# Kernel tuning notes

Hardware: AMD Instinct MI355X
Metric: run time of the kernel (lower is better)

## Reference

```python
import jax, jax.numpy as jnp
import numpy as np
import math

B, NRES, RPR = 1, 384, 3
L = NRES * RPR          # 1152 rigids
CS, CZ = 256, 128
CH, H, PQ, PV = 16, 8, 8, 12


def _ln(x, scale, bias):
    mu = jnp.mean(x, axis=-1, keepdims=True)
    var = jnp.var(x, axis=-1, keepdims=True)
    return (x - mu) * jax.lax.rsqrt(var + 1e-5) * scale + bias


def _quat_to_rot(q):
    q = q / jnp.linalg.norm(q, axis=-1, keepdims=True)
    w, x, y, z = q[..., 0], q[..., 1], q[..., 2], q[..., 3]
    r = jnp.stack([
        1 - 2 * (y * y + z * z), 2 * (x * y - w * z), 2 * (x * z + w * y),
        2 * (x * y + w * z), 1 - 2 * (x * x + z * z), 2 * (y * z - w * x),
        2 * (x * z - w * y), 2 * (y * z + w * x), 1 - 2 * (x * x + y * y),
    ], axis=-1)
    return r.reshape(q.shape[:-1] + (3, 3))


def setup_inputs() -> dict:
    key = jax.random.key(0)
    ks = jax.random.split(key, 20)
    s = jax.random.normal(ks[0], (B, L, CS), jnp.float32)
    z = jax.random.normal(ks[1], (B, NRES, NRES, CZ), jnp.float32)
    rot = _quat_to_rot(jax.random.normal(ks[2], (B, L, 4), jnp.float32))
    trans = 10.0 * jax.random.normal(ks[3], (B, L, 3), jnp.float32)
    mask = jnp.ones((B, L), jnp.float32)
    rigid_to_res_idx = jnp.broadcast_to(jnp.arange(L, dtype=jnp.int32) // RPR, (B, L))
    w = lambda k, sh: 0.02 * jax.random.normal(k, sh, jnp.float32)
    return {
        "s": s, "z": z, "rot": rot, "trans": trans, "mask": mask,
        "ln_s_scale": jnp.ones((CS,), jnp.float32), "ln_s_bias": jnp.zeros((CS,), jnp.float32),
        "ln_z_scale": jnp.ones((CZ,), jnp.float32), "ln_z_bias": jnp.zeros((CZ,), jnp.float32),
        "w_q": w(ks[4], (CS, H * CH)), "w_k": w(ks[5], (CS, H * CH)), "w_v": w(ks[6], (CS, H * CH)),
        "w_qp": w(ks[7], (CS, H * PQ * 3)), "w_kp": w(ks[8], (CS, H * PQ * 3)), "w_vp": w(ks[9], (CS, H * PV * 3)),
        "w_b": w(ks[10], (CZ, H)),
        "head_weights": jnp.full((H,), 0.5413, jnp.float32),  # softplus^-1(1)
        "w_out": w(ks[11], (H * (CH + CZ + PV * 4), CS)),
        "b_out": jnp.zeros((CS,), jnp.float32),
        "rigid_to_res_idx": rigid_to_res_idx,
    }


def reference(s, z, rot, trans, mask, ln_s_scale, ln_s_bias, ln_z_scale, ln_z_bias,
              w_q, w_k, w_v, w_qp, w_kp, w_vp, w_b, head_weights, w_out, b_out,
              rigid_to_res_idx):
    b_, l_ = s.shape[0], s.shape[1]
    idx = rigid_to_res_idx[0]                       # [L] rigid -> residue, shared over batch
    s_ln = _ln(s, ln_s_scale, ln_s_bias)            # [B,L,CS]
    z_ln = _ln(z, ln_z_scale, ln_z_bias)            # [B,N,N,CZ]

    q = (s_ln @ w_q).reshape(b_, l_, H, CH)
    k = (s_ln @ w_k).reshape(b_, l_, H, CH)
    v = (s_ln @ w_v).reshape(b_, l_, H, CH)

    # local points, then rigid-transform to global frame: x_g = R x + t
    q_p = (s_ln @ w_qp).reshape(b_, l_, H, PQ, 3)
    k_p = (s_ln @ w_kp).reshape(b_, l_, H, PQ, 3)
    v_p = (s_ln @ w_vp).reshape(b_, l_, H, PV, 3)
    t5 = trans[:, :, None, None, :]
    q_g = jnp.einsum("blij,blhpj->blhpi", rot, q_p) + t5
    k_g = jnp.einsum("blij,blhpj->blhpi", rot, k_p) + t5
    v_g = jnp.einsum("blij,blhpj->blhpi", rot, v_p) + t5

    # scalar qk term
    a = jnp.einsum("blhc,bjhc->bhlj", q, k) * math.sqrt(1.0 / (3 * CH))
    # pair bias, broadcast residue-pair -> rigid-pair
    b_res = z_ln @ w_b                                # [B,N,N,H]
    b_full = b_res[:, idx][:, :, idx]                 # [B,L,L,H]
    a = a + math.sqrt(1.0 / 3) * jnp.transpose(b_full, (0, 3, 1, 2))
    # point-distance term: ||q-k||^2 = |q|^2 + |k|^2 - 2 q.k (summed over P,3)
    hw = jax.nn.softplus(head_weights) * math.sqrt(1.0 / (3 * (PQ * 9.0 / 2)))
    qq = jnp.sum(q_g * q_g, axis=(-1, -2)).transpose(0, 2, 1)   # [B,H,L]
    kk = jnp.sum(k_g * k_g, axis=(-1, -2)).transpose(0, 2, 1)
    qk = jnp.einsum("blhpc,bjhpc->bhlj", q_g, k_g)
    d2 = qq[:, :, :, None] + kk[:, :, None, :] - 2.0 * qk
    a = a - 0.5 * d2 * hw[None, :, None, None]
    a = a + (mask[:, None, None, :] - 1.0) * 1e9
    attn = jax.nn.softmax(a, axis=-1)                 # [B,H,L,L]

    o = jnp.einsum("bhlj,bjhc->blhc", attn, v)        # [B,L,H,CH]
    o_pt_g = jnp.einsum("bhlj,bjhpc->blhpc", attn, v_g)
    # back to local frame of query rigid: R^T (x - t)
    o_pt = jnp.einsum("blji,blhpj->blhpi", rot, o_pt_g - t5)
    o_pt_norm = jnp.sqrt(jnp.sum(o_pt * o_pt, axis=-1) + 1e-8)  # [B,L,H,PV]
    # pair output: sum attention over rigids belonging to each key residue
    attn_res = attn.reshape(b_, H, l_, NRES, RPR).sum(-1)       # [B,H,L,N]
    z_l = z_ln[:, idx]                                           # [B,L,N,CZ]
    o_pair = jnp.einsum("bhln,blnc->blhc", attn_res, z_l)        # [B,L,H,CZ]

    cat = jnp.concatenate(
        [o, o_pt.reshape(b_, l_, H, PV * 3), o_pt_norm, o_pair], axis=-1
    ).reshape(b_, l_, H * (CH + PV * 4 + CZ))
    return cat @ w_out + b_out                        # [B,L,CS]
```

## Files before the change

### kernel.cpp

```cpp
#include <hip/hip_runtime.h>
#include <hip/hip_bf16.h>

#define L 1152
#define NRES 384
#define CS 256
#define CZ 128
#define H 8
#define CH 16
#define PQ 8
#define PV 12
#define PSTR 1088

#define OFF_SLN  0L
#define OFF_PROJ 294912L
#define OFF_WPK  1548288L
#define OFF_QCAT 1826816L
#define OFF_KCAT 2232320L
#define OFF_VCAT 2637824L
#define OFF_BRES 3227648L
#define OFF_MURS 4407296L
#define OFF_ATTN 4702208L
#define OFF_CAT  15319040L
#define OFF_PAV  18286592L
#define OFF_POP  21825536L
#define OFF_ARES 26544128L
#define OFF_PCAT 30083072L

__global__ __launch_bounds__(256) void k_pre(
    const float* wq, const float* wk, const float* wv,
    const float* wqp, const float* wkp, const float* wvp, float* wpack,
    const float* s, const float* lnss, const float* lnsb, float* sln,
    const float* z, const float* lnzs, const float* lnzb,
    const float* wb, float* murs, float* bres_t){
  int bx = blockIdx.x, t = threadIdx.x;
  if(bx < 256){
    int k = bx;
    for(int c=t; c<PSTR; c+=256){
      float v;
      if(c<128)        v = wq [(long)k*128 + c];
      else if(c<256)   v = wk [(long)k*128 + c-128];
      else if(c<384)   v = wv [(long)k*128 + c-256];
      else if(c<576)   v = wqp[(long)k*192 + c-384];
      else if(c<768)   v = wkp[(long)k*192 + c-576];
      else if(c<1056)  v = wvp[(long)k*288 + c-768];
      else             v = 0.f;
      wpack[(long)k*PSTR + c] = v;
    }
    return;
  }
  if(bx < 256 + L){
    int l = bx - 256;
    __shared__ float red[CS];
    float x = s[(long)l*CS + t];
    red[t] = x; __syncthreads();
    for(int st=128; st>0; st>>=1){ if(t<st) red[t]+=red[t+st]; __syncthreads(); }
    float mu = red[0] * (1.f/CS); __syncthreads();
    float d = x - mu;
    red[t] = d*d; __syncthreads();
    for(int st=128; st>0; st>>=1){ if(t<st) red[t]+=red[t+st]; __syncthreads(); }
    float var = red[0]*(1.f/CS);
    sln[(long)l*CS + t] = d*rsqrtf(var + 1e-5f)*lnss[t] + lnsb[t];
    return;
  }
  {
    long rp0 = (long)(bx - 256 - L)*32;
    int r = t>>3, part = t&7;
    long rp = rp0 + r;
    __shared__ __align__(16) float swb[8*132];
    __shared__ float SB[8][2];
    const float4* z4 = (const float4*)z;
    float4 x0 = z4[rp*32 + part*4 + 0];
    float4 x1 = z4[rp*32 + part*4 + 1];
    float4 x2 = z4[rp*32 + part*4 + 2];
    float4 x3 = z4[rp*32 + part*4 + 3];
    #pragma unroll
    for(int k2=0;k2<4;k2++){
      int e = t + k2*256; int h = e>>7, c = e&127;
      swb[h*132 + c] = lnzs[c]*wb[(long)c*8 + h];
    }
    __syncthreads();
    if(t < 64){
      int h = t>>3, seg = t&7;
      float S=0, Bv=0;
      #pragma unroll
      for(int i=0;i<16;i++){
        int c = seg*16+i;
        S  += swb[h*132+c];
        Bv += lnzb[c]*wb[(long)c*8 + h];
      }
      #pragma unroll
      for(int off=1;off<8;off<<=1){ S += __shfl_xor(S,off,64); Bv += __shfl_xor(Bv,off,64); }
      if(seg==0){ SB[h][0]=S; SB[h][1]=Bv; }
    }
    float s1 = x0.x+x0.y+x0.z+x0.w + x1.x+x1.y+x1.z+x1.w
             + x2.x+x2.y+x2.z+x2.w + x3.x+x3.y+x3.z+x3.w;
    float s2 = x0.x*x0.x+x0.y*x0.y+x0.z*x0.z+x0.w*x0.w
             + x1.x*x1.x+x1.y*x1.y+x1.z*x1.z+x1.w*x1.w
             + x2.x*x2.x+x2.y*x2.y+x2.z*x2.z+x2.w*x2.w
             + x3.x*x3.x+x3.y*x3.y+x3.z*x3.z+x3.w*x3.w;
    #pragma unroll
    for(int off=1;off<8;off<<=1){ s1 += __shfl_xor(s1,off,64); s2 += __shfl_xor(s2,off,64); }
    float mu = s1*(1.f/CZ);
    float var = s2*(1.f/CZ) - mu*mu;
    float rstd = rsqrtf(var + 1e-5f);
    if(part==0){ murs[rp*2]=mu; murs[rp*2+1]=rstd; }
    float acc[8];
    const float4* swb4 = (const float4*)swb;
    #pragma unroll
    for(int h=0;h<8;h++){
      float4 wa = swb4[h*33 + part*4 + 0];
      float4 wbv= swb4[h*33 + part*4 + 1];
      float4 wc = swb4[h*33 + part*4 + 2];
      float4 wd = swb4[h*33 + part*4 + 3];
      acc[h] = x0.x*wa.x + x0.y*wa.y + x0.z*wa.z + x0.w*wa.w
             + x1.x*wbv.x+ x1.y*wbv.y+ x1.z*wbv.z+ x1.w*wbv.w
             + x2.x*wc.x + x2.y*wc.y + x2.z*wc.z + x2.w*wc.w
             + x3.x*wd.x + x3.y*wd.y + x3.z*wd.z + x3.w*wd.w;
    }
    #pragma unroll
    for(int off=1;off<8;off<<=1){
      #pragma unroll
      for(int h=0;h<8;h++) acc[h] += __shfl_xor(acc[h],off,64);
    }
    __syncthreads();
    if(part==0){
      #pragma unroll
      for(int h=0;h<8;h++)
        bres_t[(long)h*147456 + rp] = rstd*(acc[h] - mu*SB[h][0]) + SB[h][1];
    }
  }
}

__global__ __launch_bounds__(256) void k_proj(const float* sln, const float* wpack, float* proj){
  int l0 = blockIdx.x*64, c0 = blockIdx.y*64, t = threadIdx.x;
  __shared__ float a_s[32][68];
  __shared__ __align__(16) float w_s[32][68];
  int tr = t>>4, tc = t&15;
  float4 acc[4] = {{0,0,0,0},{0,0,0,0},{0,0,0,0},{0,0,0,0}};
  for(int kc=0; kc<8; kc++){
    int k0 = kc*32;
    {
      int row = t>>2, kk0 = (t&3)*8;
      const float4* src = (const float4*)(sln + (long)(l0+row)*256 + k0 + kk0);
      float4 v0 = src[0], v1 = src[1];
      a_s[kk0+0][row]=v0.x; a_s[kk0+1][row]=v0.y; a_s[kk0+2][row]=v0.z; a_s[kk0+3][row]=v0.w;
      a_s[kk0+4][row]=v1.x; a_s[kk0+5][row]=v1.y; a_s[kk0+6][row]=v1.z; a_s[kk0+7][row]=v1.w;
    }
    #pragma unroll
    for(int kk2=0; kk2<2; kk2++){
      int kk = (t>>4) + 16*kk2;
      *(float4*)&w_s[kk][(t&15)*4] = *(const float4*)(wpack + (long)(k0+kk)*PSTR + c0 + (t&15)*4);
    }
    __syncthreads();
    #pragma unroll 8
    for(int kk=0; kk<32; kk++){
      float4 a4 = *(const float4*)&a_s[kk][tr*4];
      float4 b4 = *(const float4*)&w_s[kk][tc*4];
      acc[0].x+=a4.x*b4.x; acc[0].y+=a4.x*b4.y; acc[0].z+=a4.x*b4.z; acc[0].w+=a4.x*b4.w;
      acc[1].x+=a4.y*b4.x; acc[1].y+=a4.y*b4.y; acc[1].z+=a4.y*b4.z; acc[1].w+=a4.y*b4.w;
      acc[2].x+=a4.z*b4.x; acc[2].y+=a4.z*b4.y; acc[2].z+=a4.z*b4.z; acc[2].w+=a4.z*b4.w;
      acc[3].x+=a4.w*b4.x; acc[3].y+=a4.w*b4.y; acc[3].z+=a4.w*b4.z; acc[3].w+=a4.w*b4.w;
    }
    __syncthreads();
  }
  #pragma unroll
  for(int r=0;r<4;r++)
    *(float4*)(proj + (long)(l0 + tr*4 + r)*PSTR + c0 + tc*4) = acc[r];
}

__global__ __launch_bounds__(256) void k_rigid(const float* proj, const float* rot, const float* trans,
                        const float* mask, const float* hws,
                        float* qcat, float* kcat, float* vcat){
  int l = blockIdx.x, t = threadIdx.x;
  __shared__ float R[9], T[3], hwS[8], qgs[192], kgs[192];
  if(t<9) R[t]=rot[(long)l*9+t];
  if(t<3) T[t]=trans[(long)l*3+t];
  if(t>=16 && t<24) hwS[t-16] = log1pf(expf(hws[t-16]))*0.09622504486493764f;
  __syncthreads();
  const float* pr = proj + (long)l*PSTR;
  if(t<128){
    int h=t>>4, c=t&15;
    long base = ((long)h*L + l)*44;
    qcat[base + c] = 0.14433756729740643f * pr[t];
    kcat[base + c] = pr[128+t];
    vcat[((long)h*L + l)*64 + c] = pr[256+t];
  }
  if(t < 192){
    int h=t/24, m=t%24, p=m/3, i=m%3;
    float qa = R[i*3+0]*pr[384+h*24+p*3+0] + R[i*3+1]*pr[384+h*24+p*3+1]
             + R[i*3+2]*pr[384+h*24+p*3+2] + T[i];
    float ka = R[i*3+0]*pr[576+h*24+p*3+0] + R[i*3+1]*pr[576+h*24+p*3+1]
             + R[i*3+2]*pr[576+h*24+p*3+2] + T[i];
    qgs[t]=qa; kgs[t]=ka;
    long base = ((long)h*L + l)*44 + 16 + m;
    qcat[base] = hwS[h]*qa;
    kcat[base] = ka;
  }
  for(int it=t; it<288; it+=256){
    int h=it/36, m=it%36, p=m/3, i=m%3;
    float a = R[i*3+0]*pr[768+h*36+p*3+0] + R[i*3+1]*pr[768+h*36+p*3+1]
            + R[i*3+2]*pr[768+h*36+p*3+2] + T[i];
    vcat[((long)h*L + l)*64 + 16 + m] = a;
  }
  if(t < 96){
    int h=t/12, d=t%12;
    vcat[((long)h*L + l)*64 + 52 + d] = 0.f;
  }
  __syncthreads();
  if(t < 8){
    float qq=0, kk=0;
    #pragma unroll
    for(int m=0;m<24;m++){ qq += qgs[t*24+m]*qgs[t*24+m]; kk += kgs[t*24+m]*kgs[t*24+m]; }
    long base = ((long)t*L + l)*44;
    qcat[base + 40] = -0.5f*hwS[t]*qq;
    kcat[base + 40] = -0.5f*hwS[t]*kk + (mask[l]-1.f)*1e9f;
  }
}

__global__ __launch_bounds__(256) void k_scores(const float* qcat, const float* kcat,
                         const float* bres_t, const int* ridx, float* attn){
  int l0 = blockIdx.x*32, j0 = blockIdx.y*64, h = blockIdx.z;
  int t = threadIdx.x;
  __shared__ __align__(16) float q_s[32*44];
  __shared__ __align__(16) float k_s[64*44];
  __shared__ int rj_s[64];
  {
    const float* srcq = qcat + ((long)h*L + l0)*44;
    for(int i=t; i<32*44; i+=256) q_s[i]=srcq[i];
    const float* srck = kcat + ((long)h*L + j0)*44;
    for(int i=t; i<64*44; i+=256) k_s[i]=srck[i];
    if(t<64) rj_s[t]=ridx[j0+t];
  }
  __syncthreads();
  int a = t>>5;
  int b = t&31;
  float acc[4][2] = {{0,0},{0,0},{0,0},{0,0}};
  const float4* q4 = (const float4*)q_s;
  const float4* k4 = (const float4*)k_s;
  #pragma unroll
  for(int i=0;i<10;i++){
    float4 kA = k4[(long)b*11 + i];
    float4 kB = k4[(long)(b+32)*11 + i];
    #pragma unroll
    for(int r=0;r<4;r++){
      float4 qv = q4[(long)(a+8*r)*11 + i];
      acc[r][0] += qv.x*kA.x + qv.y*kA.y + qv.z*kA.z + qv.w*kA.w;
      acc[r][1] += qv.x*kB.x + qv.y*kB.y + qv.z*kB.z + qv.w*kB.w;
    }
  }
  float colc0 = k_s[b*44+40], colc1 = k_s[(b+32)*44+40];
  int rj0 = rj_s[b], rj1 = rj_s[b+32];
  const float* bbh = bres_t + (long)h*147456;
  #pragma unroll
  for(int r=0;r<4;r++){
    int row = a+8*r;
    float rowc = q_s[row*44+40];
    int rl = ridx[l0+row];
    const float* bb = bbh + (long)rl*NRES;
    float s0 = acc[r][0] + rowc + colc0 + 0.5773502691896258f*bb[rj0];
    float s1 = acc[r][1] + rowc + colc1 + 0.5773502691896258f*bb[rj1];
    float* arow = attn + ((long)h*L + l0+row)*L + j0;
    arow[b]    = s0;
    arow[b+32] = s1;
  }
}

__global__ __launch_bounds__(256) void k_rowstat(float* attn, float* ares){
  long row = (long)blockIdx.x*4 + (threadIdx.x>>6);
  int lane = threadIdx.x & 63;
  int w = threadIdx.x >> 6;
  __shared__ float es[4][1152];
  float* p = attn + row*L;
  float v[18];
  float m=-1e30f;
  #pragma unroll
  for(int i=0;i<18;i++){ v[i]=p[lane + i*64]; m=fmaxf(m,v[i]); }
  #pragma unroll
  for(int off=1;off<64;off<<=1) m=fmaxf(m,__shfl_xor(m,off,64));
  float s=0;
  #pragma unroll
  for(int i=0;i<18;i++){ v[i]=__expf(v[i]-m); s+=v[i]; }
  #pragma unroll
  for(int off=1;off<64;off<<=1) s+=__shfl_xor(s,off,64);
  float inv = 1.f/s;
  #pragma unroll
  for(int i=0;i<18;i++){
    float pv = v[i]*inv;
    p[lane + i*64] = pv;
    es[w][lane + i*64] = pv;
  }
  __syncthreads();
  #pragma unroll
  for(int q=0;q<6;q++){
    int n = lane + q*64;
    ares[row*NRES + n] = es[w][3*n] + es[w][3*n+1] + es[w][3*n+2];
  }
}

__global__ __launch_bounds__(256) void k_av(const float* attn, const float* vcat, float* pav){
  int lb = blockIdx.x, h = blockIdx.y, sp = blockIdx.z, t = threadIdx.x;
  int l0 = lb*64;
  __shared__ __align__(16) float a_s[64][68];
  __shared__ __align__(16) float v_s[64][68];
  int lgrp = t>>4, dgrp = t&15;
  float4 acc[4] = {{0,0,0,0},{0,0,0,0},{0,0,0,0},{0,0,0,0}};
  const float* abase = attn + ((long)h*L + l0)*L;
  int al = t>>2, jj0s = (t&3)*16;
  for(int jc=sp*3; jc<sp*3+3; jc++){
    int j0 = jc*64;
    {
      const float4* src = (const float4*)(abase + (long)al*L + j0 + jj0s);
      float4 p0 = src[0], p1 = src[1], p2 = src[2], p3 = src[3];
      a_s[jj0s+ 0][al]=p0.x; a_s[jj0s+ 1][al]=p0.y; a_s[jj0s+ 2][al]=p0.z; a_s[jj0s+ 3][al]=p0.w;
      a_s[jj0s+ 4][al]=p1.x; a_s[jj0s+ 5][al]=p1.y; a_s[jj0s+ 6][al]=p1.z; a_s[jj0s+ 7][al]=p1.w;
      a_s[jj0s+ 8][al]=p2.x; a_s[jj0s+ 9][al]=p2.y; a_s[jj0s+10][al]=p2.z; a_s[jj0s+11][al]=p2.w;
      a_s[jj0s+12][al]=p3.x; a_s[jj0s+13][al]=p3.y; a_s[jj0s+14][al]=p3.z; a_s[jj0s+15][al]=p3.w;
    }
    {
      int jj = t>>2, seg = t&3;
      const float4* src = (const float4*)(vcat + ((long)h*L + j0 + jj)*64 + seg*16);
      float4 q0=src[0], q1=src[1], q2=src[2], q3=src[3];
      float4* dst = (float4*)&v_s[jj][seg*16];
      dst[0]=q0; dst[1]=q1; dst[2]=q2; dst[3]=q3;
    }
    __syncthreads();
    #pragma unroll 8
    for(int jj=0; jj<64; jj++){
      float4 av = *(const float4*)&a_s[jj][lgrp*4];
      float4 vv = *(const float4*)&v_s[jj][dgrp*4];
      acc[0].x+=av.x*vv.x; acc[0].y+=av.x*vv.y; acc[0].z+=av.x*vv.z; acc[0].w+=av.x*vv.w;
      acc[1].x+=av.y*vv.x; acc[1].y+=av.y*vv.y; acc[1].z+=av.y*vv.z; acc[1].w+=av.y*vv.w;
      acc[2].x+=av.z*vv.x; acc[2].y+=av.z*vv.y; acc[2].z+=av.z*vv.z; acc[2].w+=av.z*vv.w;
      acc[3].x+=av.w*vv.x; acc[3].y+=av.w*vv.y; acc[3].z+=av.w*vv.z; acc[3].w+=av.w*vv.w;
    }
    __syncthreads();
  }
  #pragma unroll
  for(int r=0;r<4;r++)
    *(float4*)(pav + (((long)sp*H + h)*L + l0 + lgrp*4 + r)*64 + dgrp*4) = acc[r];
}

#define OPAIR_STEP(Z0,Z1,Z2,Z3,NB) { \
    float4 a0 = *(const float4*)&ar[0][th][NB]; \
    float4 a1 = *(const float4*)&ar[1][th][NB]; \
    float4 a2 = *(const float4*)&ar[2][th][NB]; \
    acc[0][0] += a0.x*Z0.x + a0.y*Z1.x + a0.z*Z2.x + a0.w*Z3.x; \
    acc[0][1] += a0.x*Z0.y + a0.y*Z1.y + a0.z*Z2.y + a0.w*Z3.y; \
    acc[0][2] += a0.x*Z0.z + a0.y*Z1.z + a0.z*Z2.z + a0.w*Z3.z; \
    acc[0][3] += a0.x*Z0.w + a0.y*Z1.w + a0.z*Z2.w + a0.w*Z3.w; \
    acc[1][0] += a1.x*Z0.x + a1.y*Z1.x + a1.z*Z2.x + a1.w*Z3.x; \
    acc[1][1] += a1.x*Z0.y + a1.y*Z1.y + a1.z*Z2.y + a1.w*Z3.y; \
    acc[1][2] += a1.x*Z0.z + a1.y*Z1.z + a1.z*Z2.z + a1.w*Z3.z; \
    acc[1][3] += a1.x*Z0.w + a1.y*Z1.w + a1.z*Z2.w + a1.w*Z3.w; \
    acc[2][0] += a2.x*Z0.x + a2.y*Z1.x + a2.z*Z2.x + a2.w*Z3.x; \
    acc[2][1] += a2.x*Z0.y + a2.y*Z1.y + a2.z*Z2.y + a2.w*Z3.y; \
    acc[2][2] += a2.x*Z0.z + a2.y*Z1.z + a2.z*Z2.z + a2.w*Z3.z; \
    acc[2][3] += a2.x*Z0.w + a2.y*Z1.w + a2.z*Z2.w + a2.w*Z3.w; }

__global__ __launch_bounds__(256) void k_opair(const float* ares, const float* z, const float* murs,
                        const float* sc, const int* ridx, float* po){
  int r=blockIdx.x, sp=blockIdx.y, t=threadIdx.x;
  __shared__ __align__(16) float ar[3][H][96];
  __shared__ __align__(16) float mrs[96*2];
  __shared__ float S1s[24];
  int rl = ridx[r*3];
  int n0 = sp*96;
  int tc = t&31, th = t>>5;
  const float* zbase = z + ((long)(rl*NRES + n0))*CZ + tc*4;
  float4 zc0 = *(const float4*)(zbase + 0L*CZ);
  float4 zc1 = *(const float4*)(zbase + 1L*CZ);
  float4 zc2 = *(const float4*)(zbase + 2L*CZ);
  float4 zc3 = *(const float4*)(zbase + 3L*CZ);
  for(int i=t;i<192;i+=256) mrs[i]=murs[((long)rl*NRES + n0)*2 + i];
  __syncthreads();
  for(int it=t; it<3*H*96; it+=256){
    int lo = it/(H*96);
    int rem = it - lo*(H*96);
    int h = rem/96, n = rem - h*96;
    ar[lo][h][n] = ares[((long)h*L + r*3+lo)*NRES + n0 + n] * mrs[n*2+1];
  }
  __syncthreads();
  if(t<192){
    int row=t>>3, seg=t&7;
    const float* arr = ((const float*)ar) + row*96 + seg*12;
    const float* mur = mrs + seg*24;
    float s1=0;
    #pragma unroll
    for(int q2=0;q2<12;q2++) s1 += arr[q2]*mur[q2*2];
    s1 += __shfl_xor(s1,1,64); s1 += __shfl_xor(s1,2,64); s1 += __shfl_xor(s1,4,64);
    if(seg==0) S1s[row]=s1;
  }
  __syncthreads();
  float acc[3][4]={};
  for(int nb=0; nb<88; nb+=8){
    float4 zn0 = *(const float4*)(zbase + (long)(nb+4)*CZ);
    float4 zn1 = *(const float4*)(zbase + (long)(nb+5)*CZ);
    float4 zn2 = *(const float4*)(zbase + (long)(nb+6)*CZ);
    float4 zn3 = *(const float4*)(zbase + (long)(nb+7)*CZ);
    OPAIR_STEP(zc0,zc1,zc2,zc3, nb);
    zc0 = *(const float4*)(zbase + (long)(nb+ 8)*CZ);
    zc1 = *(const float4*)(zbase + (long)(nb+ 9)*CZ);
    zc2 = *(const float4*)(zbase + (long)(nb+10)*CZ);
    zc3 = *(const float4*)(zbase + (long)(nb+11)*CZ);
    OPAIR_STEP(zn0,zn1,zn2,zn3, nb+4);
  }
  {
    float4 zn0 = *(const float4*)(zbase + 92L*CZ);
    float4 zn1 = *(const float4*)(zbase + 93L*CZ);
    float4 zn2 = *(const float4*)(zbase + 94L*CZ);
    float4 zn3 = *(const float4*)(zbase + 95L*CZ);
    OPAIR_STEP(zc0,zc1,zc2,zc3, 88);
    OPAIR_STEP(zn0,zn1,zn2,zn3, 92);
  }
  float4 sc4 = *(const float4*)(sc + tc*4);
  #pragma unroll
  for(int lo=0;lo<3;lo++){
    float s1v = S1s[lo*8+th];
    float4 o = { sc4.x*(acc[lo][0]-s1v), sc4.y*(acc[lo][1]-s1v),
                 sc4.z*(acc[lo][2]-s1v), sc4.w*(acc[lo][3]-s1v) };
    *(float4*)(po + ((long)sp*L + (long)(r*3+lo))*1024 + th*128 + tc*4) = o;
  }
}

__global__ __launch_bounds__(256) void k_post(const float* pav, const float* rot, const float* trans,
                        const float* po, const float* bi, float* cat){
  int bx = blockIdx.x, t = threadIdx.x;
  if(bx < 288){
    int lb = bx % 36, h = bx / 36;
    int l0 = lb*32;
    __shared__ __align__(16) float fin_s[32][64];
    #pragma unroll
    for(int k=0;k<2;k++){
      int fi = t + k*256;
      int l = fi>>4, c4 = fi&15;
      long base = (((long)h)*L + l0 + l)*64 + c4*4;
      float4 r = {0,0,0,0};
      #pragma unroll
      for(int p=0;p<6;p++){
        float4 a = *(const float4*)(pav + (long)p*589824 + base);
        r.x+=a.x; r.y+=a.y; r.z+=a.z; r.w+=a.w;
      }
      *(float4*)&fin_s[l][c4*4] = r;
    }
    __syncthreads();
    for(int it=t; it<32*16; it+=256){
      int l=it>>4, c=it&15;
      cat[(long)(l0+l)*1536 + h*192 + c] = fin_s[l][c];
    }
    for(int it=t; it<32*12; it+=256){
      int l=it/12, p=it%12;
      long gl = l0+l;
      float og0 = fin_s[l][16+p*3+0]-trans[gl*3+0];
      float og1 = fin_s[l][16+p*3+1]-trans[gl*3+1];
      float og2 = fin_s[l][16+p*3+2]-trans[gl*3+2];
      float* crow = cat + gl*1536 + h*192;
      float nrm=0;
      #pragma unroll
      for(int i=0;i<3;i++){
        float v = rot[gl*9+0+i]*og0 + rot[gl*9+3+i]*og1 + rot[gl*9+6+i]*og2;
        crow[16+p*3+i]=v; nrm+=v*v;
      }
      crow[52+p]=sqrtf(nrm+1e-8f);
    }
    return;
  }
  {
    int i = (bx-288)*256 + t;
    const float4* p = (const float4*)po;
    float4 a = p[i], b = p[i + 294912], c = p[i + 589824], d = p[i + 884736];
    int l = i>>8, rem = i&255;
    int h = rem>>5, c4 = rem&31;
    float4 bv = ((const float4*)bi)[c4];
    float4 r = {a.x+b.x+c.x+d.x+bv.x, a.y+b.y+c.y+d.y+bv.y,
                a.z+b.z+c.z+d.z+bv.z, a.w+b.w+c.w+d.w+bv.w};
    ((float4*)cat)[(long)l*384 + h*48 + 16 + c4] = r;
  }
}

__global__ __launch_bounds__(256) void k_final(const float* cat, const float* wout, float* pcat){
  int l0 = blockIdx.x*64, c0 = blockIdx.y*64, kp = blockIdx.z, t = threadIdx.x;
  __shared__ __align__(16) float a_s[64][68];
  __shared__ __align__(16) float w_s[64][68];
  int lgrp = t>>4, cgrp = t&15;
  float4 acc[4] = {{0,0,0,0},{0,0,0,0},{0,0,0,0},{0,0,0,0}};
  int al = t>>2, ks0 = (t&3)*16;
  for(int kc=0; kc<3; kc++){
    int k0 = kp*192 + kc*64;
    {
      const float4* src = (const float4*)(cat + (long)(l0+al)*1536 + k0 + ks0);
      float4 p0 = src[0], p1 = src[1], p2 = src[2], p3 = src[3];
      a_s[ks0+ 0][al]=p0.x; a_s[ks0+ 1][al]=p0.y; a_s[ks0+ 2][al]=p0.z; a_s[ks0+ 3][al]=p0.w;
      a_s[ks0+ 4][al]=p1.x; a_s[ks0+ 5][al]=p1.y; a_s[ks0+ 6][al]=p1.z; a_s[ks0+ 7][al]=p1.w;
      a_s[ks0+ 8][al]=p2.x; a_s[ks0+ 9][al]=p2.y; a_s[ks0+10][al]=p2.z; a_s[ks0+11][al]=p2.w;
      a_s[ks0+12][al]=p3.x; a_s[ks0+13][al]=p3.y; a_s[ks0+14][al]=p3.z; a_s[ks0+15][al]=p3.w;
    }
    {
      int kk = t>>2, seg = t&3;
      const float4* src = (const float4*)(wout + (long)(k0+kk)*256 + c0 + seg*16);
      float4 q0=src[0], q1=src[1], q2=src[2], q3=src[3];
      float4* dst = (float4*)&w_s[kk][seg*16];
      dst[0]=q0; dst[1]=q1; dst[2]=q2; dst[3]=q3;
    }
    __syncthreads();
    #pragma unroll 8
    for(int kk=0; kk<64; kk++){
      float4 av = *(const float4*)&a_s[kk][lgrp*4];
      float4 wv = *(const float4*)&w_s[kk][cgrp*4];
      acc[0].x+=av.x*wv.x; acc[0].y+=av.x*wv.y; acc[0].z+=av.x*wv.z; acc[0].w+=av.x*wv.w;
      acc[1].x+=av.y*wv.x; acc[1].y+=av.y*wv.y; acc[1].z+=av.y*wv.z; acc[1].w+=av.y*wv.w;
      acc[2].x+=av.z*wv.x; acc[2].y+=av.z*wv.y; acc[2].z+=av.z*wv.z; acc[2].w+=av.z*wv.w;
      acc[3].x+=av.w*wv.x; acc[3].y+=av.w*wv.y; acc[3].z+=av.w*wv.z; acc[3].w+=av.w*wv.w;
    }
    __syncthreads();
  }
  #pragma unroll
  for(int r=0;r<4;r++)
    *(float4*)(pcat + ((long)kp*L + l0 + lgrp*4 + r)*256 + c0 + cgrp*4) = acc[r];
}

__global__ __launch_bounds__(256) void k_redout(const float* pcat, const float* bout, float* out){
  int i = blockIdx.x*256 + threadIdx.x;
  const float4* p = (const float4*)pcat;
  float4 bv = ((const float4*)bout)[i&63];
  float4 r = bv;
  #pragma unroll
  for(int p8=0;p8<8;p8++){
    float4 a = p[i + (long)p8*73728];
    r.x+=a.x; r.y+=a.y; r.z+=a.z; r.w+=a.w;
  }
  ((float4*)out)[i] = r;
}

extern "C" void kernel_launch(void* const* d_in, const int* in_sizes, int n_in,
                              void* d_out, int out_size, void* d_ws, size_t ws_size,
                              hipStream_t stream) {
  const float* s      = (const float*)d_in[0];
  const float* z      = (const float*)d_in[1];
  const float* rot    = (const float*)d_in[2];
  const float* trans  = (const float*)d_in[3];
  const float* mask   = (const float*)d_in[4];
  const float* lnss   = (const float*)d_in[5];
  const float* lnsb   = (const float*)d_in[6];
  const float* lnzs   = (const float*)d_in[7];
  const float* lnzb   = (const float*)d_in[8];
  const float* wq     = (const float*)d_in[9];
  const float* wk     = (const float*)d_in[10];
  const float* wv     = (const float*)d_in[11];
  const float* wqp    = (const float*)d_in[12];
  const float* wkp    = (const float*)d_in[13];
  const float* wvp    = (const float*)d_in[14];
  const float* wb     = (const float*)d_in[15];
  const float* hws    = (const float*)d_in[16];
  const float* wout   = (const float*)d_in[17];
  const float* bout   = (const float*)d_in[18];
  const int*  ridx    = (const int*)d_in[19];

  float* ws  = (float*)d_ws;
  float* out = (float*)d_out;

  float* sln  = ws + OFF_SLN;
  float* proj = ws + OFF_PROJ;
  float* wpk  = ws + OFF_WPK;
  float* qcat = ws + OFF_QCAT;
  float* kcat = ws + OFF_KCAT;
  float* vcat = ws + OFF_VCAT;
  float* bres = ws + OFF_BRES;
  float* murs = ws + OFF_MURS;
  float* attn = ws + OFF_ATTN;
  float* cat  = ws + OFF_CAT;
  float* pcat = ws + OFF_PCAT;
  float* pav  = ws + OFF_PAV;
  float* po   = ws + OFF_POP;
  float* ares = ws + OFF_ARES;

  k_pre<<<dim3(256 + L + NRES*NRES/32), dim3(256), 0, stream>>>(
      wq, wk, wv, wqp, wkp, wvp, wpk,
      s, lnss, lnsb, sln,
      z, lnzs, lnzb, wb, murs, bres);
  k_proj<<<dim3(18,17), dim3(256), 0, stream>>>(sln, wpk, proj);
  k_rigid<<<dim3(L), dim3(256), 0, stream>>>(proj, rot, trans, mask, hws, qcat, kcat, vcat);
  k_scores<<<dim3(L/32, L/64, H), dim3(256), 0, stream>>>(qcat, kcat, bres, ridx, attn);
  k_rowstat<<<dim3(H*L/4), dim3(256), 0, stream>>>(attn, ares);
  k_av<<<dim3(L/64, H, 6), dim3(256), 0, stream>>>(attn, vcat, pav);
  k_opair<<<dim3(NRES, 4), dim3(256), 0, stream>>>(ares, z, murs, lnzs, ridx, po);
  k_post<<<dim3(288 + 1152), dim3(256), 0, stream>>>(pav, rot, trans, po, lnzb, cat);
  k_final<<<dim3(L/64, 4, 8), dim3(256), 0, stream>>>(cat, wout, pcat);
  k_redout<<<dim3(288), dim3(256), 0, stream>>>(pcat, bout, out);
}
```

Before: 309.1 us.

## Transpose q/k layout and use 4x4 register-tiled score kernel with staged pair bias

Stores the concatenated q and k features channel-major so the score kernel can load transposed tiles and compute a 4x4 outer-product micro-tile per thread over a 32x128 block, writing float4 rows. The pair bias block for the covered residues is staged in shared memory, and the residue index is computed as j/3 instead of read from the index array. This cuts shared-memory traffic per FMA and scattered global bias gathers, but it hardcodes three rigids per residue and makes the rigid kernel's stores strided.

```diff
diff --git a/kernel.cpp b/kernel.cpp
--- a/kernel.cpp
+++ b/kernel.cpp
@@ -180,9 +180,8 @@
   const float* pr = proj + (long)l*PSTR;
   if(t<128){
     int h=t>>4, c=t&15;
-    long base = ((long)h*L + l)*44;
-    qcat[base + c] = 0.14433756729740643f * pr[t];
-    kcat[base + c] = pr[128+t];
+    qcat[((long)h*44 + c)*L + l] = 0.14433756729740643f * pr[t];
+    kcat[((long)h*44 + c)*L + l] = pr[128+t];
     vcat[((long)h*L + l)*64 + c] = pr[256+t];
   }
   if(t < 192){
@@ -192,9 +191,8 @@
     float ka = R[i*3+0]*pr[576+h*24+p*3+0] + R[i*3+1]*pr[576+h*24+p*3+1]
              + R[i*3+2]*pr[576+h*24+p*3+2] + T[i];
     qgs[t]=qa; kgs[t]=ka;
-    long base = ((long)h*L + l)*44 + 16 + m;
-    qcat[base] = hwS[h]*qa;
-    kcat[base] = ka;
+    qcat[((long)h*44 + 16 + m)*L + l] = hwS[h]*qa;
+    kcat[((long)h*44 + 16 + m)*L + l] = ka;
   }
   for(int it=t; it<288; it+=256){
     int h=it/36, m=it%36, p=m/3, i=m%3;
@@ -211,57 +209,66 @@
     float qq=0, kk=0;
     #pragma unroll
     for(int m=0;m<24;m++){ qq += qgs[t*24+m]*qgs[t*24+m]; kk += kgs[t*24+m]*kgs[t*24+m]; }
-    long base = ((long)t*L + l)*44;
-    qcat[base + 40] = -0.5f*hwS[t]*qq;
-    kcat[base + 40] = -0.5f*hwS[t]*kk + (mask[l]-1.f)*1e9f;
+    qcat[((long)t*44 + 40)*L + l] = -0.5f*hwS[t]*qq;
+    kcat[((long)t*44 + 40)*L + l] = -0.5f*hwS[t]*kk + (mask[l]-1.f)*1e9f;
   }
 }
 
 __global__ __launch_bounds__(256) void k_scores(const float* qcat, const float* kcat,
-                         const float* bres_t, const int* ridx, float* attn){
-  int l0 = blockIdx.x*32, j0 = blockIdx.y*64, h = blockIdx.z;
+                         const float* bres_t, float* attn){
+  int l0 = blockIdx.x*32, j0 = blockIdx.y*128, h = blockIdx.z;
   int t = threadIdx.x;
-  __shared__ __align__(16) float q_s[32*44];
-  __shared__ __align__(16) float k_s[64*44];
-  __shared__ int rj_s[64];
+  __shared__ __align__(16) float q_t[44*36];
+  __shared__ __align__(16) float k_t[44*132];
+  __shared__ float bp[12*44];
+  int rl0 = l0/3, rj0 = j0/3;
   {
-    const float* srcq = qcat + ((long)h*L + l0)*44;
-    for(int i=t; i<32*44; i+=256) q_s[i]=srcq[i];
-    const float* srck = kcat + ((long)h*L + j0)*44;
-    for(int i=t; i<64*44; i+=256) k_s[i]=srck[i];
-    if(t<64) rj_s[t]=ridx[j0+t];
-  }
-  __syncthreads();
-  int a = t>>5;
-  int b = t&31;
-  float acc[4][2] = {{0,0},{0,0},{0,0},{0,0}};
-  const float4* q4 = (const float4*)q_s;
-  const float4* k4 = (const float4*)k_s;
-  #pragma unroll
-  for(int i=0;i<10;i++){
-    float4 kA = k4[(long)b*11 + i];
-    float4 kB = k4[(long)(b+32)*11 + i];
-    #pragma unroll
-    for(int r=0;r<4;r++){
-      float4 qv = q4[(long)(a+8*r)*11 + i];
-      acc[r][0] += qv.x*kA.x + qv.y*kA.y + qv.z*kA.z + qv.w*kA.w;
-      acc[r][1] += qv.x*kB.x + qv.y*kB.y + qv.z*kB.z + qv.w*kB.w;
-    }
-  }
-  float colc0 = k_s[b*44+40], colc1 = k_s[(b+32)*44+40];
-  int rj0 = rj_s[b], rj1 = rj_s[b+32];
-  const float* bbh = bres_t + (long)h*147456;
+    const float* srcq = qcat + (long)h*44*L + l0;
+    for(int i=t; i<44*32; i+=256){
+      int c = i>>5, ll = i&31;
+      q_t[c*36 + ll] = srcq[(long)c*L + ll];
+    }
+    const float* srck = kcat + (long)h*44*L + j0;
+    for(int i=t; i<44*128; i+=256){
+      int c = i>>7, jj = i&127;
+      k_t[c*132 + jj] = srck[(long)c*L + jj];
+    }
+    const float* bb = bres_t + (long)h*147456;
+    for(int i=t; i<12*44; i+=256){
+      int r = i/44, c = i-r*44;
+      int rr = rl0+r, cc = rj0+c;
+      bp[i] = (rr<NRES && cc<NRES) ? bb[(long)rr*NRES + cc] : 0.f;
+    }
+  }
+  __syncthreads();
+  int lg = t>>5, jg = t&31;
+  float acc[4][4] = {};
+  #pragma unroll 4
+  for(int c=0;c<40;c++){
+    float4 qv = *(const float4*)&q_t[c*36 + lg*4];
+    float4 kv = *(const float4*)&k_t[c*132 + jg*4];
+    acc[0][0]+=qv.x*kv.x; acc[0][1]+=qv.x*kv.y; acc[0][2]+=qv.x*kv.z; acc[0][3]+=qv.x*kv.w;
+    acc[1][0]+=qv.y*kv.x; acc[1][1]+=qv.y*kv.y; acc[1][2]+=qv.y*kv.z; acc[1][3]+=qv.y*kv.w;
+    acc[2][0]+=qv.z*kv.x; acc[2][1]+=qv.z*kv.y; acc[2][2]+=qv.z*kv.z; acc[2][3]+=qv.z*kv.w;
+    acc[3][0]+=qv.w*kv.x; acc[3][1]+=qv.w*kv.y; acc[3][2]+=qv.w*kv.z; acc[3][3]+=qv.w*kv.w;
+  }
+  float4 colc = *(const float4*)&k_t[40*132 + jg*4];
+  int jb = j0 + jg*4;
+  int rj0i = (jb  )/3 - rj0;
+  int rj1i = (jb+1)/3 - rj0;
+  int rj2i = (jb+2)/3 - rj0;
+  int rj3i = (jb+3)/3 - rj0;
   #pragma unroll
   for(int r=0;r<4;r++){
-    int row = a+8*r;
-    float rowc = q_s[row*44+40];
-    int rl = ridx[l0+row];
-    const float* bb = bbh + (long)rl*NRES;
-    float s0 = acc[r][0] + rowc + colc0 + 0.5773502691896258f*bb[rj0];
-    float s1 = acc[r][1] + rowc + colc1 + 0.5773502691896258f*bb[rj1];
-    float* arow = attn + ((long)h*L + l0+row)*L + j0;
-    arow[b]    = s0;
-    arow[b+32] = s1;
+    int row = lg*4+r;
+    float rowc = q_t[40*36 + row];
+    const float* bpr = &bp[((l0+row)/3 - rl0)*44];
+    float4 o;
+    o.x = acc[r][0] + rowc + colc.x + 0.5773502691896258f*bpr[rj0i];
+    o.y = acc[r][1] + rowc + colc.y + 0.5773502691896258f*bpr[rj1i];
+    o.z = acc[r][2] + rowc + colc.z + 0.5773502691896258f*bpr[rj2i];
+    o.w = acc[r][3] + rowc + colc.w + 0.5773502691896258f*bpr[rj3i];
+    *(float4*)(attn + ((long)h*L + l0+row)*L + jb) = o;
   }
 }
 
@@ -579,7 +586,7 @@
       z, lnzs, lnzb, wb, murs, bres);
   k_proj<<<dim3(18,17), dim3(256), 0, stream>>>(sln, wpk, proj);
   k_rigid<<<dim3(L), dim3(256), 0, stream>>>(proj, rot, trans, mask, hws, qcat, kcat, vcat);
-  k_scores<<<dim3(L/32, L/64, H), dim3(256), 0, stream>>>(qcat, kcat, bres, ridx, attn);
+  k_scores<<<dim3(L/32, L/128, H), dim3(256), 0, stream>>>(qcat, kcat, bres, attn);
   k_rowstat<<<dim3(H*L/4), dim3(256), 0, stream>>>(attn, ares);
   k_av<<<dim3(L/64, H, 6), dim3(256), 0, stream>>>(attn, vcat, pav);
   k_opair<<<dim3(NRES, 4), dim3(256), 0, stream>>>(ares, z, murs, lnzs, ridx, po);
```

Result: no change. 305.6 us (-1.1%).
